# Optimization experiments

Measured on AMD Instinct MI355X. Metric: run time of the kernel, lower is better.

The kernel has to match this reference:

```python
import jax, jax.numpy as jnp
import numpy as np

B, S, D, H, E, K = 2, 2048, 1024, 8, 4, 2
DH = D // H  # 128


def setup_inputs() -> dict:
    key = jax.random.key(0)
    ks = jax.random.split(key, 9)
    std = 1.0 / np.sqrt(D)
    return {
        "q_src": jax.random.normal(ks[0], (B, S, D), jnp.float32),
        "k_src": jax.random.normal(ks[1], (B, S, D), jnp.float32),
        "v_src": jax.random.normal(ks[2], (B, S, D), jnp.float32),
        "Wq": jax.random.normal(ks[3], (H * DH, D), jnp.float32) * std,
        "Wk": jax.random.normal(ks[4], (H * DH, D), jnp.float32) * std,
        "Wv": jax.random.normal(ks[5], (H, E, D, DH), jnp.float32) * std,   # per-head, per-expert V proj
        "Wo": jax.random.normal(ks[6], (H, E, DH, D), jnp.float32) * (1.0 / np.sqrt(H * DH)),
        "sel_v": jax.random.normal(ks[7], (H * E, D), jnp.float32) * std,   # V-expert router
        "sel_o": jax.random.normal(ks[8], (H * E, D), jnp.float32) * std,   # O-expert router
    }


def reference(q_src, k_src, v_src, Wq, Wk, Wv, Wo, sel_v, sel_o):
    s = DH ** -0.25  # scale.sqrt() applied to both q and k -> combined 1/sqrt(d_head)

    q = (q_src @ Wq.T * s).reshape(B, S, H, DH).transpose(0, 2, 1, 3)  # [B,H,S,DH]
    k = (k_src @ Wk.T * s).reshape(B, S, H, DH).transpose(0, 2, 1, 3)

    # --- V expert routing: sigmoid gate + top-k over experts, per head ---
    gv_all = jax.nn.sigmoid((k_src @ sel_v.T).reshape(B, S, H, E))
    gv, iv = jax.lax.top_k(gv_all, K)                                  # [B,S,H,K]
    # per-expert V projection (equiv. to CVMM grouped-GEMM), then gather selected experts
    v_all = jnp.einsum('bsd,hedk->bshek', v_src, Wv)                   # [B,S,H,E,DH]
    v = (jnp.take_along_axis(v_all, iv[..., None], axis=3) * gv[..., None]).sum(3)
    v = v.transpose(0, 2, 1, 3)                                        # [B,H,S,DH]

    # --- attention (mask=None; base class attend() is abstract, plain SDPA) ---
    scores = jnp.einsum('bhqd,bhkd->bhqk', q, k)
    att = jax.nn.softmax(scores, axis=-1)
    res = jnp.einsum('bhqk,bhkd->bhqd', att, v).transpose(0, 2, 1, 3)  # [B,S,H,DH]

    # --- O expert routing: weighted sum over heads and selected output experts ---
    go_all = jax.nn.sigmoid((q_src @ sel_o.T).reshape(B, S, H, E))
    go, io = jax.lax.top_k(go_all, K)                                  # [B,S,H,K]
    gd = (go[..., None] * jax.nn.one_hot(io, E, dtype=res.dtype)).sum(-2)  # dense gates [B,S,H,E]
    gated = res[:, :, :, None, :] * gd[..., None]                      # [B,S,H,E,DH]
    out = jnp.einsum('bshed,hedo->bso', gated, Wo)                     # [B,S,D]
    return out
```

## Files before the change

### kernel.cpp

```cpp
#include <hip/hip_runtime.h>

#define BB 2
#define SS 2048
#define DD 1024
#define HH 8
#define EE 4
#define DHH 128
#define RR (BB*SS)

typedef __attribute__((ext_vector_type(8))) short short8;
typedef __attribute__((ext_vector_type(4))) short short4v;
typedef __attribute__((ext_vector_type(4))) float f32x4;

__device__ __forceinline__ float b2f(short x) {
    unsigned u = ((unsigned)(unsigned short)x) << 16;
    return __uint_as_float(u);
}
__device__ __forceinline__ short f2bf(float f) {
    unsigned u = __float_as_uint(f);
    unsigned r = (u + 0x7fffu + ((u >> 16) & 1u)) >> 16;
    return (short)(unsigned short)r;
}

__device__ __forceinline__ void gl_lds16(const short* g, short* l) {
    __builtin_amdgcn_global_load_lds(
        (const __attribute__((address_space(1))) unsigned int*)g,
        (__attribute__((address_space(3))) unsigned int*)l,
        16, 0, 0);
}

template <bool BF16_OUT>
__device__ __forceinline__ void gemm16_body(
    short* As, short* Bs,
    const short* __restrict__ A, const short* __restrict__ Bm, void* __restrict__ Cv,
    int Kd, int lda, int ldb, int ldc, float alpha, int bm0, int bn0)
{
    const int t = threadIdx.x;
    const int lane = t & 63, wave = t >> 6;
    const int lm = lane & 15, quad = lane >> 4;
    const int wm = (wave >> 1) * 64, wn = (wave & 1) * 64;
    f32x4 acc[4][4] = {};

    const int srow = t >> 2, scol = (t & 3) * 8;
    const short* Ag = A + (long)(bm0 + srow) * lda + scol;
    const short* Bg = Bm + (long)(bn0 + srow) * ldb + scol;
    const long ldaH = (long)lda * 64, ldbH = (long)ldb * 64;
    short* Asd = As + srow * 32 + scol;
    short* Bsd = Bs + srow * 32 + scol;

    for (int k0 = 0; k0 < Kd; k0 += 32) {
        __syncthreads();
        gl_lds16(Ag + k0,        Asd);
        gl_lds16(Ag + k0 + ldaH, Asd + 64 * 32);
        gl_lds16(Bg + k0,        Bsd);
        gl_lds16(Bg + k0 + ldbH, Bsd + 64 * 32);
        __syncthreads();

        short8 af[4], bf[4];
#pragma unroll
        for (int i = 0; i < 4; i++)
            af[i] = *(const short8*)&As[(wm + i * 16 + lm) * 32 + quad * 8];
#pragma unroll
        for (int j = 0; j < 4; j++)
            bf[j] = *(const short8*)&Bs[(wn + j * 16 + lm) * 32 + quad * 8];
#pragma unroll
        for (int i = 0; i < 4; i++)
#pragma unroll
            for (int j = 0; j < 4; j++)
                acc[i][j] = __builtin_amdgcn_mfma_f32_16x16x32_bf16(
                    af[i], bf[j], acc[i][j], 0, 0, 0);
    }
#pragma unroll
    for (int i = 0; i < 4; i++) {
#pragma unroll
        for (int j = 0; j < 4; j++) {
            int n = bn0 + wn + j * 16 + lm;
#pragma unroll
            for (int r = 0; r < 4; r++) {
                int m = bm0 + wm + i * 16 + quad * 4 + r;
                float v = acc[i][j][r] * alpha;
                if (BF16_OUT) ((short*)Cv)[(long)m * ldc + n] = f2bf(v);
                else          ((float*)Cv)[(long)m * ldc + n] = v;
            }
        }
    }
}

__global__ __launch_bounds__(256)
void shc_gemm_bt16(const short* __restrict__ A, const short* __restrict__ Bm,
                   void* __restrict__ Cv, int Kd, int lda, int ldb, int ldc,
                   float alpha)
{
    __shared__ short As[128 * 32];
    __shared__ short Bs[128 * 32];
    gemm16_body<true>(As, Bs, A, Bm, Cv, Kd, lda, ldb, ldc, alpha,
                      blockIdx.y * 128, blockIdx.x * 128);
}

__global__ __launch_bounds__(256)
void shc_gemm_qk(const short* __restrict__ Qs, const short* __restrict__ Ks,
                 const short* __restrict__ Wq16, const short* __restrict__ Wk16,
                 short* __restrict__ Qo, short* __restrict__ Ko, float alpha)
{
    __shared__ short As[128 * 32];
    __shared__ short Bs[128 * 32];
    if (blockIdx.z == 0)
        gemm16_body<true>(As, Bs, Qs, Wq16, Qo, 1024, 1024, 1024, 1024,
                          alpha, blockIdx.y * 128, blockIdx.x * 128);
    else
        gemm16_body<true>(As, Bs, Ks, Wk16, Ko, 1024, 1024, 1024, 1024,
                          alpha, blockIdx.y * 128, blockIdx.x * 128);
}

__global__ __launch_bounds__(256)
void shc_gemm_out(const short* __restrict__ X, const short* __restrict__ WoT,
                  float* __restrict__ out, float* __restrict__ P1)
{
    __shared__ short As[128 * 32];
    __shared__ short Bs[128 * 32];
    const int koff = blockIdx.z * 2048;
    float* C = blockIdx.z ? P1 : out;
    gemm16_body<false>(As, Bs, X + koff, WoT + koff, C,
                       2048, 4096, 4096, 1024, 1.0f,
                       blockIdx.y * 128, blockIdx.x * 128);
}

__global__ __launch_bounds__(256)
void shc_add(float* __restrict__ out, const float* __restrict__ P1)
{
    long i = ((long)blockIdx.x * 256 + threadIdx.x) * 4;
    f32x4 a = *(const f32x4*)(out + i);
    f32x4 b = *(const f32x4*)(P1 + i);
#pragma unroll
    for (int j = 0; j < 4; j++) a[j] += b[j];
    *(f32x4*)(out + i) = a;
}

__global__ __launch_bounds__(256)
void shc_cvt3(const float* __restrict__ a, const float* __restrict__ b,
              const float* __restrict__ c, short* __restrict__ oa,
              short* __restrict__ ob, short* __restrict__ oc)
{
    const float* src = blockIdx.z == 0 ? a : (blockIdx.z == 1 ? b : c);
    short* dst       = blockIdx.z == 0 ? oa : (blockIdx.z == 1 ? ob : oc);
    long i = ((long)blockIdx.x * 256 + threadIdx.x) * 8;
    f32x4 f0 = *(const f32x4*)(src + i);
    f32x4 f1 = *(const f32x4*)(src + i + 4);
    short8 o;
#pragma unroll
    for (int j = 0; j < 4; j++) {
        o[j]     = f2bf(f0[j]);
        o[4 + j] = f2bf(f1[j]);
    }
    *(short8*)(dst + i) = o;
}

__global__ __launch_bounds__(256)
void shc_gates4(const float* __restrict__ q_src, const float* __restrict__ k_src,
                const float* __restrict__ sel_v, const float* __restrict__ sel_o,
                float* __restrict__ gv_d, float* __restrict__ go_d)
{
    const int t = threadIdx.x, lane = t & 63, wave = t >> 6;
    const int bid = blockIdx.x;
    const int s = bid & 1;
    const int r0 = (bid >> 1) * 8 + wave * 2;
    const float* srcb = s ? q_src : k_src;
    const float* selb = s ? sel_o : sel_v;

    double S0[16], S1[16];
#pragma unroll
    for (int i = 0; i < 4; i++) {
        f32x4 v0 = *(const f32x4*)(srcb + (long)r0 * 1024 + lane * 16 + i * 4);
        f32x4 v1 = *(const f32x4*)(srcb + (long)(r0 + 1) * 1024 + lane * 16 + i * 4);
#pragma unroll
        for (int j = 0; j < 4; j++) {
            S0[i * 4 + j] = (double)v0[j];
            S1[i * 4 + j] = (double)v1[j];
        }
    }

    float myv = 0.f;
#pragma unroll 2
    for (int o = 0; o < 32; ++o) {
        f32x4 W[4];
#pragma unroll
        for (int i = 0; i < 4; i++)
            W[i] = *(const f32x4*)(selb + o * 1024 + lane * 16 + i * 4);
        double a0 = 0.0, a1 = 0.0;
#pragma unroll
        for (int i = 0; i < 4; i++)
#pragma unroll
            for (int j = 0; j < 4; j++) {
                double w = (double)W[i][j];
                a0 += S0[i * 4 + j] * w;
                a1 += S1[i * 4 + j] * w;
            }
        a0 += __shfl_xor(a0, 1);  a1 += __shfl_xor(a1, 1);
        a0 += __shfl_xor(a0, 2);  a1 += __shfl_xor(a1, 2);
        a0 += __shfl_xor(a0, 4);  a1 += __shfl_xor(a1, 4);
        a0 += __shfl_xor(a0, 8);  a1 += __shfl_xor(a1, 8);
        a0 += __shfl_xor(a0, 16); a1 += __shfl_xor(a1, 16);
        double tcross = (lane < 32) ? a1 : a0;
        double u = __shfl_xor(tcross, 32);
        double tot = ((lane < 32) ? a0 : a1) + u;
        myv = ((lane & 31) == o) ? (float)tot : myv;
    }

    float sg = 1.f / (1.f + __expf(-myv));
    float g1 = __shfl_xor(sg, 1);
    float g2 = __shfl_xor(sg, 2);
    float g3 = __shfl_xor(sg, 3);
    const int e = lane & 3;
    int rank = 0;
    rank += (g1 > sg) || (g1 == sg && (e ^ 1) < e);
    rank += (g2 > sg) || (g2 == sg && (e ^ 2) < e);
    rank += (g3 > sg) || (g3 == sg && (e ^ 3) < e);
    const long row = r0 + (lane >> 5);
    float* outp = (s ? go_d : gv_d) + row * 32 + (lane & 31);
    *outp = (rank < 2) ? sg : 0.f;
}

__global__ __launch_bounds__(256)
void shc_transpose_w(const float* __restrict__ Wv, short* __restrict__ WvT,
                     const float* __restrict__ Wo, short* __restrict__ WoT)
{
    __shared__ float Ls[32][33];
    const int t = threadIdx.x;
    const int rr = t >> 3, cc = (t & 7) * 4;
    const int bid = blockIdx.x;
    if (bid < 4096) {
        const int dhT = bid & 3, dT = (bid >> 2) & 31, he = bid >> 7;
        const int d0 = dT * 32, dh0 = dhT * 32;
        f32x4 vin = *(const f32x4*)(Wv + (long)(he * 1024 + d0 + rr) * 128 + dh0 + cc);
#pragma unroll
        for (int j = 0; j < 4; j++) Ls[rr][cc + j] = vin[j];
        __syncthreads();
        short4v ov;
#pragma unroll
        for (int j = 0; j < 4; j++) ov[j] = f2bf(Ls[cc + j][rr]);
        *(short4v*)(WvT + (long)(he * 128 + dh0 + rr) * 1024 + d0 + cc) = ov;
    } else {
        const int b2 = bid - 4096;
        const int oT = b2 & 31, kT = b2 >> 5;
        const int k0 = kT * 32, o0 = oT * 32;
        f32x4 vin = *(const f32x4*)(Wo + (long)(k0 + rr) * 1024 + o0 + cc);
#pragma unroll
        for (int j = 0; j < 4; j++) Ls[rr][cc + j] = vin[j];
        __syncthreads();
        short4v ov;
#pragma unroll
        for (int j = 0; j < 4; j++) ov[j] = f2bf(Ls[cc + j][rr]);
        *(short4v*)(WoT + (long)(o0 + rr) * 4096 + k0 + cc) = ov;
    }
}

__global__ __launch_bounds__(256)
void shc_combine_vt(const short* __restrict__ v_all, const float* __restrict__ gv_d,
                    short* __restrict__ Vt)
{
    __shared__ short Ls[64 * 136];
    const int t = threadIdx.x;
    const int blk = blockIdx.x;
    const int st = blk & 31, h = (blk >> 5) & 7, b = blk >> 8;
    const int s0 = st * 64;
    const int sl = t >> 2, dh0 = (t & 3) * 32;
    const long row = (long)(b * SS) + s0 + sl;
    const float* g = gv_d + row * 32 + h * 4;
    float g0 = g[0], g1 = g[1], g2 = g[2], g3 = g[3];
    const short* va = v_all + row * 4096 + h * 512;
#pragma unroll
    for (int j = 0; j < 4; j++) {
        int dh = dh0 + j * 8;
        short8 e0 = *(const short8*)(va + 0 * 128 + dh);
        short8 e1 = *(const short8*)(va + 1 * 128 + dh);
        short8 e2 = *(const short8*)(va + 2 * 128 + dh);
        short8 e3 = *(const short8*)(va + 3 * 128 + dh);
        short8 outv;
#pragma unroll
        for (int i = 0; i < 8; i++)
            outv[i] = f2bf(g0 * b2f(e0[i]) + g1 * b2f(e1[i])
                         + g2 * b2f(e2[i]) + g3 * b2f(e3[i]));
        *(short8*)&Ls[sl * 136 + dh] = outv;
    }
    __syncthreads();
    const int dh = t >> 1, sc0 = (t & 1) * 32;
    short* op = Vt + ((long)(b * HH + h) * DHH + dh) * SS + s0 + sc0;
#pragma unroll
    for (int j = 0; j < 4; j++) {
        short8 ov;
#pragma unroll
        for (int i = 0; i < 8; i++)
            ov[i] = Ls[(sc0 + j * 8 + i) * 136 + dh];
        *(short8*)(op + j * 8) = ov;
    }
}

#define NEG10L2E -14.426950408889634f
__global__ __launch_bounds__(256)
void shc_attn_mfma(const short* __restrict__ Q, const short* __restrict__ Kg,
                   const short* __restrict__ Vt, const float* __restrict__ go_d,
                   short* __restrict__ X)
{
    __shared__ __align__(16) char smem[40960];
    short* Ks = (short*)smem;
    short* Vs = (short*)(smem + 16384);
    const int t = threadIdx.x;
    const int lane = t & 63, wave = t >> 6;
    const int lm = lane & 15, quad = lane >> 4;
    short* Pw = (short*)(smem + 32768) + wave * 16 * 64;
    const int bid = blockIdx.x;
    const int blk = ((bid & 7) << 6) | (bid >> 3);
    const int qt = blk & 31, h = (blk >> 5) & 7, b = blk >> 8;
    const int q0 = qt * 64 + wave * 16;
    const short* Qb = Q + ((long)(b * SS) + q0) * DD + h * DHH;
    const short* Kb = Kg + (long)(b * SS) * DD + h * DHH;
    const short* Vb = Vt + (long)(b * HH + h) * DHH * SS;

    short8 af[4];
#pragma unroll
    for (int c = 0; c < 4; c++)
        af[c] = *(const short8*)(Qb + (long)lm * DD + c * 32 + quad * 8);

    f32x4 o_acc[8] = {};
    float l_lane[4] = {0.f, 0.f, 0.f, 0.f};

    const int ksrow = t >> 2, kscol = (t & 3) * 32;
    const int vsrow = t >> 1, vscol = (t & 1) * 32;
    const int kswz = (ksrow & 7) << 3;
    const int vswz = (vsrow & 7) << 3;
    const int lmswz = (lm & 7) << 3;

    short8 kv[4], vv[4];
#pragma unroll
    for (int j = 0; j < 4; j++) {
        kv[j] = *(const short8*)(Kb + (long)ksrow * DD + kscol + j * 8);
        vv[j] = *(const short8*)(Vb + (long)vsrow * SS + vscol + j * 8);
    }

    for (int kt = 0; kt < SS / 64; ++kt) {
        __syncthreads();
#pragma unroll
        for (int j = 0; j < 4; j++) {
            *(short8*)&Ks[ksrow * 128 + ((kscol + j * 8) ^ kswz)] = kv[j];
            *(short8*)&Vs[vsrow * 64  + ((vscol + j * 8) ^ vswz)] = vv[j];
        }
        __syncthreads();

        const int ktn = (kt + 1) & 31;
#pragma unroll
        for (int j = 0; j < 4; j++) {
            kv[j] = *(const short8*)(Kb + (long)(ktn * 64 + ksrow) * DD + kscol + j * 8);
            vv[j] = *(const short8*)(Vb + (long)vsrow * SS + ktn * 64 + vscol + j * 8);
        }

        __builtin_amdgcn_s_setprio(1);
#pragma unroll
        for (int f = 0; f < 4; f++) {
            f32x4 acc = {NEG10L2E, NEG10L2E, NEG10L2E, NEG10L2E};
#pragma unroll
            for (int c = 0; c < 4; c++) {
                short8 bf = *(const short8*)&Ks[(f * 16 + lm) * 128
                                                + ((c * 32 + quad * 8) ^ lmswz)];
                acc = __builtin_amdgcn_mfma_f32_16x16x32_bf16(af[c], bf, acc, 0, 0, 0);
            }
#pragma unroll
            for (int r = 0; r < 4; r++) {
                float p = exp2f(acc[r]);
                l_lane[r] += p;
                const int pr = quad * 4 + r;
                Pw[pr * 64 + ((f * 16 + lm) ^ ((pr & 7) << 3))] = f2bf(p);
            }
        }

        short8 ap0 = *(const short8*)&Pw[lm * 64 + ((quad * 8) ^ lmswz)];
        short8 ap1 = *(const short8*)&Pw[lm * 64 + ((32 + quad * 8) ^ lmswz)];
#pragma unroll
        for (int d = 0; d < 8; d++) {
            short8 bv0 = *(const short8*)&Vs[(d * 16 + lm) * 64 + ((quad * 8) ^ lmswz)];
            short8 bv1 = *(const short8*)&Vs[(d * 16 + lm) * 64 + ((32 + quad * 8) ^ lmswz)];
            o_acc[d] = __builtin_amdgcn_mfma_f32_16x16x32_bf16(ap0, bv0, o_acc[d], 0, 0, 0);
            o_acc[d] = __builtin_amdgcn_mfma_f32_16x16x32_bf16(ap1, bv1, o_acc[d], 0, 0, 0);
        }
        __builtin_amdgcn_s_setprio(0);
    }

    float inv_r[4];
#pragma unroll
    for (int r = 0; r < 4; r++) {
        float l = l_lane[r];
        l += __shfl_xor(l, 1);
        l += __shfl_xor(l, 2);
        l += __shfl_xor(l, 4);
        l += __shfl_xor(l, 8);
        inv_r[r] = 1.f / l;
    }

    __syncthreads();
    float* Of = (float*)smem;
#pragma unroll
    for (int r = 0; r < 4; r++) {
#pragma unroll
        for (int d = 0; d < 8; d++)
            Of[(wave * 16 + quad * 4 + r) * 132 + d * 16 + lm] = o_acc[d][r] * inv_r[r];
    }
    __syncthreads();
    const int xr = t >> 2, xc0 = (t & 3) * 8;
    const long grow = (long)(b * SS) + qt * 64 + xr;
    const float* go4 = go_d + grow * 32 + h * 4;
    float gg[4] = {go4[0], go4[1], go4[2], go4[3]};
    short* Xp = X + grow * 4096 + h * 512;
#pragma unroll
    for (int e = 0; e < 4; e++) {
#pragma unroll
        for (int j = 0; j < 4; j++) {
            int c = xc0 + 32 * j;
            f32x4 f0 = *(const f32x4*)&Of[xr * 132 + c];
            f32x4 f1 = *(const f32x4*)&Of[xr * 132 + c + 4];
            short8 s;
#pragma unroll
            for (int i = 0; i < 4; i++) {
                s[i]     = f2bf(f0[i] * gg[e]);
                s[4 + i] = f2bf(f1[i] * gg[e]);
            }
            *(short8*)(Xp + e * 128 + c) = s;
        }
    }
}

extern "C" void kernel_launch(void* const* d_in, const int* in_sizes, int n_in,
                              void* d_out, int out_size, void* d_ws, size_t ws_size,
                              hipStream_t stream)
{
    const float* q_src = (const float*)d_in[0];
    const float* k_src = (const float*)d_in[1];
    const float* v_src = (const float*)d_in[2];
    const float* Wq    = (const float*)d_in[3];
    const float* Wk    = (const float*)d_in[4];
    const float* Wv    = (const float*)d_in[5];
    const float* Wo    = (const float*)d_in[6];
    const float* sel_v = (const float*)d_in[7];
    const float* sel_o = (const float*)d_in[8];
    float* out = (float*)d_out;
    char* ws = (char*)d_ws;

    short* Qb16 = (short*)(ws + 0);
    short* Kb16 = (short*)(ws + 8388608);
    short* Vtg  = (short*)(ws + 16777216);
    short* Vs16 = (short*)(ws + 16777216);
    short* Vall = (short*)(ws + 25165824);
    short* X    = (short*)(ws + 25165824);
    short* Wq16 = (short*)(ws + 25165824);
    short* Wk16 = (short*)(ws + 27262976);
    float* P1   = (float*)(ws + 58720256);
    short* Qs16 = (short*)(ws + 58720256);
    short* Ks16 = (short*)(ws + 67108864);
    short* WvT  = (short*)(ws + 75497472);
    short* WoT  = (short*)(ws + 83886080);
    float* GVd  = (float*)(ws + 92274688);
    float* GOd  = (float*)(ws + 92798976);

    const float s_scale = 0.29730177875068026f * 1.2011224087864498f;

    dim3 blk(256);
    shc_cvt3<<<dim3(2048, 1, 3), blk, 0, stream>>>(q_src, k_src, v_src, Qs16, Ks16, Vs16);
    shc_cvt3<<<dim3(512, 1, 2), blk, 0, stream>>>(Wq, Wk, Wk, Wq16, Wk16, Wk16);
    shc_gemm_qk<<<dim3(8, 32, 2), blk, 0, stream>>>(Qs16, Ks16, Wq16, Wk16, Qb16, Kb16, s_scale);
    shc_gates4<<<1024, blk, 0, stream>>>(q_src, k_src, sel_v, sel_o, GVd, GOd);
    shc_transpose_w<<<8192, blk, 0, stream>>>(Wv, WvT, Wo, WoT);
    shc_gemm_bt16<<<dim3(32, 32), blk, 0, stream>>>(Vs16, WvT, Vall, 1024, 1024, 1024, 4096, 1.0f);
    shc_combine_vt<<<512, blk, 0, stream>>>(Vall, GVd, Vtg);
    shc_attn_mfma<<<512, blk, 0, stream>>>(Qb16, Kb16, Vtg, GOd, X);
    shc_gemm_out<<<dim3(8, 32, 2), blk, 0, stream>>>(X, WoT, out, P1);
    shc_add<<<4096, blk, 0, stream>>>(out, P1);
}
```

Baseline: 407.4 us.

## Load K/V tiles directly to LDS instead of register-prefetch pipeline

Replaces the register-staged prefetch of the next K and V tiles with direct global-to-LDS loads (gl_lds16) issued at the top of each iteration, with a swizzled layout computed per lane. It also drops the block-index remapping and the s_setprio hints. This removes register pressure and the extra register-to-LDS stores, but loses the overlap of next-tile global loads with MFMA compute, since loads now sit between barriers with no double buffering.

Result: slower. 416.5 us (+2.2%).

```diff
diff --git a/kernel.cpp b/kernel.cpp
--- a/kernel.cpp
+++ b/kernel.cpp
@@ -307,9 +307,8 @@
     const int t = threadIdx.x;
     const int lane = t & 63, wave = t >> 6;
     const int lm = lane & 15, quad = lane >> 4;
-    short* Pw = (short*)(smem + 32768) + wave * 16 * 64;
-    const int bid = blockIdx.x;
-    const int blk = ((bid & 7) << 6) | (bid >> 3);
+    short* Pw = (short*)(smem + 32768) + wave * 1024;
+    const int blk = blockIdx.x;
     const int qt = blk & 31, h = (blk >> 5) & 7, b = blk >> 8;
     const int q0 = qt * 64 + wave * 16;
     const short* Qb = Q + ((long)(b * SS) + q0) * DD + h * DHH;
@@ -324,36 +323,26 @@
     f32x4 o_acc[8] = {};
     float l_lane[4] = {0.f, 0.f, 0.f, 0.f};
 
-    const int ksrow = t >> 2, kscol = (t & 3) * 32;
-    const int vsrow = t >> 1, vscol = (t & 1) * 32;
-    const int kswz = (ksrow & 7) << 3;
-    const int vswz = (vsrow & 7) << 3;
     const int lmswz = (lm & 7) << 3;
-
-    short8 kv[4], vv[4];
-#pragma unroll
-    for (int j = 0; j < 4; j++) {
-        kv[j] = *(const short8*)(Kb + (long)ksrow * DD + kscol + j * 8);
-        vv[j] = *(const short8*)(Vb + (long)vsrow * SS + vscol + j * 8);
-    }
+    const int w16 = wave * 16, w32 = wave * 32;
+
+    const int rK = lane >> 4;
+    const int colK = ((lane & 15) * 8) ^ (rK << 3);
+    const int rV = lane >> 3;
+    const int colV = ((lane & 7) * 8) ^ (rV << 3);
 
     for (int kt = 0; kt < SS / 64; ++kt) {
         __syncthreads();
 #pragma unroll
-        for (int j = 0; j < 4; j++) {
-            *(short8*)&Ks[ksrow * 128 + ((kscol + j * 8) ^ kswz)] = kv[j];
-            *(short8*)&Vs[vsrow * 64  + ((vscol + j * 8) ^ vswz)] = vv[j];
-        }
-        __syncthreads();
-
-        const int ktn = (kt + 1) & 31;
-#pragma unroll
-        for (int j = 0; j < 4; j++) {
-            kv[j] = *(const short8*)(Kb + (long)(ktn * 64 + ksrow) * DD + kscol + j * 8);
-            vv[j] = *(const short8*)(Vb + (long)vsrow * SS + ktn * 64 + vscol + j * 8);
-        }
-
-        __builtin_amdgcn_s_setprio(1);
+        for (int i = 0; i < 4; i++) {
+            const short* kg = Kb + (long)(kt * 64 + w16 + i * 4 + rK) * DD
+                              + (colK ^ ((i & 1) << 5));
+            gl_lds16(kg, Ks + (w16 + i * 4) * 128);
+            const short* vg = Vb + (long)(w32 + i * 8 + rV) * SS + kt * 64 + colV;
+            gl_lds16(vg, Vs + (w32 + i * 8) * 64);
+        }
+        __syncthreads();
+
 #pragma unroll
         for (int f = 0; f < 4; f++) {
             f32x4 acc = {NEG10L2E, NEG10L2E, NEG10L2E, NEG10L2E};
@@ -381,7 +370,6 @@
             o_acc[d] = __builtin_amdgcn_mfma_f32_16x16x32_bf16(ap0, bv0, o_acc[d], 0, 0, 0);
             o_acc[d] = __builtin_amdgcn_mfma_f32_16x16x32_bf16(ap1, bv1, o_acc[d], 0, 0, 0);
         }
-        __builtin_amdgcn_s_setprio(0);
     }
 
     float inv_r[4];
@@ -401,7 +389,7 @@
     for (int r = 0; r < 4; r++) {
 #pragma unroll
         for (int d = 0; d < 8; d++)
-            Of[(wave * 16 + quad * 4 + r) * 132 + d * 16 + lm] = o_acc[d][r] * inv_r[r];
+            Of[(w16 + quad * 4 + r) * 132 + d * 16 + lm] = o_acc[d][r] * inv_r[r];
     }
     __syncthreads();
     const int xr = t >> 2, xc0 = (t & 3) * 8;
```
